# Kernel optimization log

Hardware: AMD Instinct MI355X
Metric: run time of the kernel (lower is better)

Reference implementation:

```python
import jax, jax.numpy as jnp
import numpy as np


def setup_inputs() -> dict:
    key = jax.random.key(0)
    k1, k2, k3, k4 = jax.random.split(key, 4)
    B, H, N, D = 4, 16, 2048, 128
    return {
        "q": jax.random.normal(k1, (B, H, N, D), dtype=jnp.float32),
        "k": jax.random.normal(k2, (B, H, N, D), dtype=jnp.float32),
        "v": jax.random.normal(k3, (B, H, N, D), dtype=jnp.float32),
        "g": jax.random.normal(k4, (B, H, N, 1), dtype=jnp.float32),
    }


def reference(q, k, v, g):
    """GLA recurrence: S_t = l_t * S_{t-1} + (1 - l_t) * k_t v_t^T; o_t = q_t S_t."""
    scale = 1.0
    B, H, N, D = q.shape
    lambd = jax.nn.sigmoid(g)                      # [B,H,N,1]
    qs = q * scale
    # time-major for scan: [N,B,H,...]
    qt = jnp.moveaxis(qs, 2, 0)
    kt = jnp.moveaxis(k, 2, 0)
    vt = jnp.moveaxis(v, 2, 0)
    lt = jnp.moveaxis(lambd, 2, 0)[..., None]      # [N,B,H,1,1]
    S0 = jnp.zeros((B, H, D, D), dtype=q.dtype)

    def step(S, inp):
        q_t, k_t, v_t, l_t = inp
        kv = jnp.einsum('bhd,bhe->bhde', k_t, v_t)  # rank-1 update per head
        S = l_t * S + (1.0 - l_t) * kv
        o = jnp.einsum('bhd,bhde->bhe', q_t, S)
        return S, o

    _, outs = jax.lax.scan(step, S0, (qt, kt, vt, lt))  # outs: [N,B,H,D]
    return jnp.moveaxis(outs, 0, 2)                     # [B,H,N,D]
```

## Files before the change

kernel.cpp:

```cpp
#include <hip/hip_runtime.h>

#define NTOK 2048
#define DD   128
#define CHK  64
#define PCH  16
#define EW   32

typedef __attribute__((ext_vector_type(8))) short bf16x8;
typedef __attribute__((ext_vector_type(4))) float f32x4;
typedef unsigned short u16;

#define MFMA(a,b,c) __builtin_amdgcn_mfma_f32_16x16x32_bf16(a,b,c,0,0,0)

#define SBAR() do{ __builtin_amdgcn_sched_barrier(0); \
  asm volatile("s_waitcnt lgkmcnt(0)" ::: "memory"); \
  __builtin_amdgcn_s_barrier(); \
  __builtin_amdgcn_sched_barrier(0); }while(0)
#define VWAIT() do{ asm volatile("s_waitcnt vmcnt(0)" ::: "memory"); \
  __builtin_amdgcn_sched_barrier(0); }while(0)

__device__ __forceinline__ u16 f2bf(float f){
  union { float f; unsigned u; } x; x.f = f;
  return (u16)((x.u + 0x7fffu + ((x.u >> 16) & 1u)) >> 16);
}
__device__ __forceinline__ int swz(int r, int c, int re){
  int b = (r*re + c)*2;
  return b ^ ((r & 7) << 4);
}
__device__ __forceinline__ void lds_w1(u16* a, int r, int c, int re, u16 v){
  *(u16*)((char*)a + swz(r,c,re)) = v;
}
__device__ __forceinline__ void lds_w4(u16* a, int r, int c, int re, ushort4 v){
  *(ushort4*)((char*)a + swz(r,c,re)) = v;
}
__device__ __forceinline__ bf16x8 lds_r8(const u16* a, int r, int c, int re){
  return *(const bf16x8*)((const char*)a + swz(r,c,re));
}

__global__ __launch_bounds__(256) void gla_part(
    const float* __restrict__ Qg, const float* __restrict__ Kg,
    const float* __restrict__ Vg, const float* __restrict__ Gg,
    float* __restrict__ Og, float* __restrict__ Smid, float* __restrict__ Bpre)
{
  __shared__ u16 sKh [CHK*DD];
  __shared__ u16 sKhT[DD*CHK];
  __shared__ u16 sVT [EW*CHK];
  __shared__ u16 sST [EW*DD];
  __shared__ u16 sPb [CHK*CHK];

  const int tid = threadIdx.x;
  const int w = tid >> 6, l = tid & 63, lr = l & 15, lh = l >> 4;
  const int gid  = blockIdx.x;
  const int head = (gid & 7) | (((gid >> 6) & 7) << 3);
  const int e0   = ((gid >> 3) & 3) * EW;
  const int part = (gid >> 5) & 1;
  const int tbase = part * (PCH*CHK);

  const float* Qh = Qg + (size_t)head*NTOK*DD;
  const float* Kh = Kg + (size_t)head*NTOK*DD;
  const float* Vh = Vg + (size_t)head*NTOK*DD;
  const float* Gh = Gg + (size_t)head*NTOK;
  float* Oh = Og + (size_t)head*NTOK*DD;

  f32x4 S00 = {}, S01 = {}, S10 = {}, S11 = {};
  float4 kt[2][4];
  float4 vpre[2], qpre[8];
  float gst;

  const int q4 = (tid >> 4) * 4;
  const int j0 = tid & 15;

  auto loads = [&](int c){
    const int t0 = tbase + c*CHK;
    gst = Gh[t0 + l];
    #pragma unroll
    for (int t=0;t<2;++t){
      const float* kp = Kh + (size_t)(t0 + q4)*DD + (j0 + 16*t)*4;
      #pragma unroll
      for (int r=0;r<4;++r) kt[t][r] = *(const float4*)(kp + r*DD);
    }
    const float* vp = Vh + (size_t)(t0 + (tid>>2))*DD + e0 + 4*(tid&3);
    #pragma unroll
    for (int i=0;i<2;++i) vpre[i] = *(const float4*)(vp + 16*i);
    const float* qp = Qh + (size_t)(t0 + w*16 + lr)*DD + lh*8;
    #pragma unroll
    for (int i=0;i<4;++i){
      qpre[2*i]   = *(const float4*)(qp + 32*i);
      qpre[2*i+1] = *(const float4*)(qp + 32*i + 4);
    }
  };

  float cklr, cq, scc, bl63;
  auto scan = [&](){
    float li = 1.f/(1.f + expf(-gst));
    float x  = log2f(li);
    #pragma unroll
    for (int off=1; off<64; off<<=1){
      float y = __shfl_up(x, off, 64);
      if (l >= off) x += y;
    }
    bl63 = __shfl(x, 63, 64);
    scc  = exp2f(bl63);
    cq   = exp2f(__shfl(x, w*16 + lr, 64));
    cklr = exp2f(-x) * (1.f - li);
  };

  loads(0);
  scan();
  float bsum = 0.f;
  if (part == 1 && e0 == 0 && tid == 0) Bpre[head*PCH] = 0.f;

  for (int c=0; c<PCH; ++c){
    SBAR();
    VWAIT();

    {
      const float cs0 = __shfl(cklr, q4+0, 64);
      const float cs1 = __shfl(cklr, q4+1, 64);
      const float cs2 = __shfl(cklr, q4+2, 64);
      const float cs3 = __shfl(cklr, q4+3, 64);
      #pragma unroll
      for (int t=0;t<2;++t){
        const int d0 = (j0 + 16*t)*4;
        ushort4 r0 = make_ushort4(f2bf(kt[t][0].x*cs0), f2bf(kt[t][0].y*cs0), f2bf(kt[t][0].z*cs0), f2bf(kt[t][0].w*cs0));
        ushort4 r1 = make_ushort4(f2bf(kt[t][1].x*cs1), f2bf(kt[t][1].y*cs1), f2bf(kt[t][1].z*cs1), f2bf(kt[t][1].w*cs1));
        ushort4 r2 = make_ushort4(f2bf(kt[t][2].x*cs2), f2bf(kt[t][2].y*cs2), f2bf(kt[t][2].z*cs2), f2bf(kt[t][2].w*cs2));
        ushort4 r3 = make_ushort4(f2bf(kt[t][3].x*cs3), f2bf(kt[t][3].y*cs3), f2bf(kt[t][3].z*cs3), f2bf(kt[t][3].w*cs3));
        lds_w4(sKh, q4+0, d0, DD, r0);
        lds_w4(sKh, q4+1, d0, DD, r1);
        lds_w4(sKh, q4+2, d0, DD, r2);
        lds_w4(sKh, q4+3, d0, DD, r3);
        lds_w4(sKhT, d0+0, q4, CHK, make_ushort4(r0.x, r1.x, r2.x, r3.x));
        lds_w4(sKhT, d0+1, q4, CHK, make_ushort4(r0.y, r1.y, r2.y, r3.y));
        lds_w4(sKhT, d0+2, q4, CHK, make_ushort4(r0.z, r1.z, r2.z, r3.z));
        lds_w4(sKhT, d0+3, q4, CHK, make_ushort4(r0.w, r1.w, r2.w, r3.w));
      }
    }
    {
      const int srow = tid >> 2;
      #pragma unroll
      for (int i=0;i<2;++i){
        float4 vf = vpre[i];
        int e = 4*((tid & 3) + 4*i);
        lds_w1(sVT, e+0, srow, CHK, f2bf(vf.x));
        lds_w1(sVT, e+1, srow, CHK, f2bf(vf.y));
        lds_w1(sVT, e+2, srow, CHK, f2bf(vf.z));
        lds_w1(sVT, e+3, srow, CHK, f2bf(vf.w));
      }
    }
    {
      const int dbase = w*32 + lh*4;
      lds_w4(sST, lr,    dbase,      DD, make_ushort4(f2bf(S00[0]), f2bf(S00[1]), f2bf(S00[2]), f2bf(S00[3])));
      lds_w4(sST, 16+lr, dbase,      DD, make_ushort4(f2bf(S01[0]), f2bf(S01[1]), f2bf(S01[2]), f2bf(S01[3])));
      lds_w4(sST, lr,    dbase + 16, DD, make_ushort4(f2bf(S10[0]), f2bf(S10[1]), f2bf(S10[2]), f2bf(S10[3])));
      lds_w4(sST, 16+lr, dbase + 16, DD, make_ushort4(f2bf(S11[0]), f2bf(S11[1]), f2bf(S11[2]), f2bf(S11[3])));
    }
    bf16x8 qA[4];
    #pragma unroll
    for (int ks=0;ks<4;++ks){
      float4 a = qpre[2*ks], b = qpre[2*ks+1];
      bf16x8 t;
      t[0]=(short)f2bf(a.x*cq); t[1]=(short)f2bf(a.y*cq);
      t[2]=(short)f2bf(a.z*cq); t[3]=(short)f2bf(a.w*cq);
      t[4]=(short)f2bf(b.x*cq); t[5]=(short)f2bf(b.y*cq);
      t[6]=(short)f2bf(b.z*cq); t[7]=(short)f2bf(b.w*cq);
      qA[ks] = t;
    }
    if (c+1 < PCH) loads(c+1);
    SBAR();

    f32x4 oacc0 = {}, oacc1 = {};
    f32x4 p0 = {}, p1 = {}, p2 = {}, p3 = {};
    #pragma unroll
    for (int ks=0;ks<4;++ks){
      const int kk = ks*32 + lh*8;
      bf16x8 a = qA[ks];
      oacc0 = MFMA(a, lds_r8(sST, lr,    kk, DD), oacc0);
      oacc1 = MFMA(a, lds_r8(sST, 16+lr, kk, DD), oacc1);
      p0 = MFMA(a, lds_r8(sKh, lr,    kk, DD), p0);
      p1 = MFMA(a, lds_r8(sKh, 16+lr, kk, DD), p1);
      p2 = MFMA(a, lds_r8(sKh, 32+lr, kk, DD), p2);
      p3 = MFMA(a, lds_r8(sKh, 48+lr, kk, DD), p3);
    }
    {
      const int t = w*16 + lh*4;
      #pragma unroll
      for (int r=0;r<4;++r){
        int tt = t + r;
        lds_w1(sPb, tt, lr,    CHK, f2bf((lr    <= tt) ? p0[r] : 0.f));
        lds_w1(sPb, tt, 16+lr, CHK, f2bf((16+lr <= tt) ? p1[r] : 0.f));
        lds_w1(sPb, tt, 32+lr, CHK, f2bf((32+lr <= tt) ? p2[r] : 0.f));
        lds_w1(sPb, tt, 48+lr, CHK, f2bf((48+lr <= tt) ? p3[r] : 0.f));
      }
    }
    asm volatile("s_waitcnt lgkmcnt(0)" ::: "memory");
    __builtin_amdgcn_sched_barrier(0);

    #pragma unroll
    for (int k2=0;k2<2;++k2){
      const int kk = k2*32 + lh*8;
      bf16x8 vb0 = lds_r8(sVT, lr,    kk, CHK);
      bf16x8 vb1 = lds_r8(sVT, 16+lr, kk, CHK);
      bf16x8 pa  = lds_r8(sPb, w*16 + lr, kk, CHK);
      oacc0 = MFMA(pa, vb0, oacc0);
      oacc1 = MFMA(pa, vb1, oacc1);
      bf16x8 ka0 = lds_r8(sKhT, w*32 + lr,      kk, CHK);
      bf16x8 ka1 = lds_r8(sKhT, w*32 + 16 + lr, kk, CHK);
      S00 = MFMA(ka0, vb0, S00);
      S01 = MFMA(ka0, vb1, S01);
      S10 = MFMA(ka1, vb0, S10);
      S11 = MFMA(ka1, vb1, S11);
    }
    #pragma unroll
    for (int r=0;r<4;++r){ S00[r]*=scc; S01[r]*=scc; S10[r]*=scc; S11[r]*=scc; }

    {
      float* op = Oh + (size_t)(tbase + c*CHK + w*16 + lh*4)*DD + e0;
      #pragma unroll
      for (int r=0;r<4;++r){
        op[r*DD + lr]      = oacc0[r];
        op[r*DD + 16 + lr] = oacc1[r];
      }
    }
    if (c+1 < PCH){
      if (part == 1){
        bsum += bl63;
        if (e0 == 0 && tid == 0) Bpre[head*PCH + c + 1] = bsum;
      }
      scan();
    }
  }

  if (part == 0){
    float* sm = Smid + (size_t)head*DD*DD + e0;
    const int dbase = w*32 + lh*4;
    #pragma unroll
    for (int r=0;r<4;++r){
      sm[(size_t)(dbase + r)*DD + lr]           = S00[r];
      sm[(size_t)(dbase + r)*DD + 16 + lr]      = S01[r];
      sm[(size_t)(dbase + 16 + r)*DD + lr]      = S10[r];
      sm[(size_t)(dbase + 16 + r)*DD + 16 + lr] = S11[r];
    }
  }
}

__global__ __launch_bounds__(256) void gla_fix(
    const float* __restrict__ Qg, const float* __restrict__ Gg,
    float* __restrict__ Og, const float* __restrict__ Smid,
    const float* __restrict__ Bpre)
{
  __shared__ u16 sS[DD*DD];
  const int tid = threadIdx.x;
  const int w = tid >> 6, l = tid & 63, lr = l & 15, lh = l >> 4;
  const int head = blockIdx.x >> 4, c = blockIdx.x & 15;
  const int t0 = PCH*CHK + c*CHK;

  {
    const int d = tid >> 1, eb = (tid & 1)*64;
    const float* sp = Smid + (size_t)head*DD*DD + (size_t)d*DD + eb;
    #pragma unroll
    for (int j=0;j<16;++j){
      float4 f = *(const float4*)(sp + 4*j);
      lds_w1(sS, eb + 4*j + 0, d, DD, f2bf(f.x));
      lds_w1(sS, eb + 4*j + 1, d, DD, f2bf(f.y));
      lds_w1(sS, eb + 4*j + 2, d, DD, f2bf(f.z));
      lds_w1(sS, eb + 4*j + 3, d, DD, f2bf(f.w));
    }
  }
  float gst = Gg[(size_t)head*NTOK + t0 + l];
  float li = 1.f/(1.f + expf(-gst));
  float x  = log2f(li);
  #pragma unroll
  for (int off=1; off<64; off<<=1){
    float y = __shfl_up(x, off, 64);
    if (l >= off) x += y;
  }
  const float cq = exp2f(__shfl(x, w*16 + lr, 64) + Bpre[head*PCH + c]);

  bf16x8 qA[4];
  const float* qp = Qg + (size_t)head*NTOK*DD + (size_t)(t0 + w*16 + lr)*DD + lh*8;
  #pragma unroll
  for (int ks=0;ks<4;++ks){
    float4 a = *(const float4*)(qp + ks*32);
    float4 b = *(const float4*)(qp + ks*32 + 4);
    bf16x8 t;
    t[0]=(short)f2bf(a.x*cq); t[1]=(short)f2bf(a.y*cq);
    t[2]=(short)f2bf(a.z*cq); t[3]=(short)f2bf(a.w*cq);
    t[4]=(short)f2bf(b.x*cq); t[5]=(short)f2bf(b.y*cq);
    t[6]=(short)f2bf(b.z*cq); t[7]=(short)f2bf(b.w*cq);
    qA[ks] = t;
  }
  __syncthreads();

  f32x4 o0={},o1={},o2={},o3={},o4={},o5={},o6={},o7={};
  #pragma unroll
  for (int ks=0;ks<4;++ks){
    const int kk = ks*32 + lh*8;
    bf16x8 a = qA[ks];
    o0 = MFMA(a, lds_r8(sS, lr,      kk, DD), o0);
    o1 = MFMA(a, lds_r8(sS, 16+lr,   kk, DD), o1);
    o2 = MFMA(a, lds_r8(sS, 32+lr,   kk, DD), o2);
    o3 = MFMA(a, lds_r8(sS, 48+lr,   kk, DD), o3);
    o4 = MFMA(a, lds_r8(sS, 64+lr,   kk, DD), o4);
    o5 = MFMA(a, lds_r8(sS, 80+lr,   kk, DD), o5);
    o6 = MFMA(a, lds_r8(sS, 96+lr,   kk, DD), o6);
    o7 = MFMA(a, lds_r8(sS, 112+lr,  kk, DD), o7);
  }
  float* op = Og + (size_t)head*NTOK*DD + (size_t)(t0 + w*16 + lh*4)*DD;
  #pragma unroll
  for (int r=0;r<4;++r){
    op[r*DD + lr]       += o0[r];
    op[r*DD + 16 + lr]  += o1[r];
    op[r*DD + 32 + lr]  += o2[r];
    op[r*DD + 48 + lr]  += o3[r];
    op[r*DD + 64 + lr]  += o4[r];
    op[r*DD + 80 + lr]  += o5[r];
    op[r*DD + 96 + lr]  += o6[r];
    op[r*DD + 112 + lr] += o7[r];
  }
}

extern "C" void kernel_launch(void* const* d_in, const int* in_sizes, int n_in,
                              void* d_out, int out_size, void* d_ws, size_t ws_size,
                              hipStream_t stream)
{
  const float* q = (const float*)d_in[0];
  const float* k = (const float*)d_in[1];
  const float* v = (const float*)d_in[2];
  const float* g = (const float*)d_in[3];
  float* out = (float*)d_out;
  float* Smid = (float*)d_ws;
  float* Bpre = (float*)((char*)d_ws + (size_t)64*DD*DD*4);

  gla_part<<<dim3(512),  dim3(256), 0, stream>>>(q, k, v, g, out, Smid, Bpre);
  gla_fix <<<dim3(1024), dim3(256), 0, stream>>>(q, g, out, Smid, Bpre);
}
```

Before: 140.6 us.

## Split sequence into four parts and combine partial states in fixup

New measurement: 177.9 us. +26.5%, slower.

```diff
diff --git a/kernel.cpp b/kernel.cpp
--- a/kernel.cpp
+++ b/kernel.cpp
@@ -1,10 +1,12 @@
 #include <hip/hip_runtime.h>
 
 #define NTOK 2048
-#define DD   128
-#define CHK  64
-#define PCH  16
-#define EW   32
+#define DD    128
+#define CHK   64
+#define NPART 4
+#define PCH   8
+#define EW    32
+#define SEL   16384
 
 typedef __attribute__((ext_vector_type(8))) short bf16x8;
 typedef __attribute__((ext_vector_type(4))) float f32x4;
@@ -40,7 +42,8 @@
 __global__ __launch_bounds__(256) void gla_part(
     const float* __restrict__ Qg, const float* __restrict__ Kg,
     const float* __restrict__ Vg, const float* __restrict__ Gg,
-    float* __restrict__ Og, float* __restrict__ Smid, float* __restrict__ Bpre)
+    float* __restrict__ Og, float* __restrict__ Umid,
+    float* __restrict__ Btot, float* __restrict__ Bpre)
 {
   __shared__ u16 sKh [CHK*DD];
   __shared__ u16 sKhT[DD*CHK];
@@ -51,9 +54,9 @@
   const int tid = threadIdx.x;
   const int w = tid >> 6, l = tid & 63, lr = l & 15, lh = l >> 4;
   const int gid  = blockIdx.x;
-  const int head = (gid & 7) | (((gid >> 6) & 7) << 3);
+  const int head = (gid & 7) | (((gid >> 7) & 7) << 3);
   const int e0   = ((gid >> 3) & 3) * EW;
-  const int part = (gid >> 5) & 1;
+  const int part = (gid >> 5) & 3;
   const int tbase = part * (PCH*CHK);
 
   const float* Qh = Qg + (size_t)head*NTOK*DD;
@@ -108,7 +111,7 @@
   loads(0);
   scan();
   float bsum = 0.f;
-  if (part == 1 && e0 == 0 && tid == 0) Bpre[head*PCH] = 0.f;
+  if (e0 == 0 && tid == 0) Bpre[head*(NPART*PCH) + part*PCH] = 0.f;
 
   for (int c=0; c<PCH; ++c){
     SBAR();
@@ -223,16 +226,15 @@
       }
     }
     if (c+1 < PCH){
-      if (part == 1){
-        bsum += bl63;
-        if (e0 == 0 && tid == 0) Bpre[head*PCH + c + 1] = bsum;
-      }
+      bsum += bl63;
+      if (e0 == 0 && tid == 0) Bpre[head*(NPART*PCH) + part*PCH + c + 1] = bsum;
       scan();
     }
   }
-
-  if (part == 0){
-    float* sm = Smid + (size_t)head*DD*DD + e0;
+  bsum += bl63;
+
+  if (part < 3){
+    float* sm = Umid + ((size_t)head*3 + part)*SEL + e0;
     const int dbase = w*32 + lh*4;
     #pragma unroll
     for (int r=0;r<4;++r){
@@ -242,29 +244,44 @@
       sm[(size_t)(dbase + 16 + r)*DD + 16 + lr] = S11[r];
     }
   }
+  if ((part == 1 || part == 2) && e0 == 0 && tid == 0)
+    Btot[head*NPART + part] = bsum;
 }
 
 __global__ __launch_bounds__(256) void gla_fix(
     const float* __restrict__ Qg, const float* __restrict__ Gg,
-    float* __restrict__ Og, const float* __restrict__ Smid,
-    const float* __restrict__ Bpre)
+    float* __restrict__ Og, const float* __restrict__ Umid,
+    const float* __restrict__ Btot, const float* __restrict__ Bpre)
 {
   __shared__ u16 sS[DD*DD];
   const int tid = threadIdx.x;
   const int w = tid >> 6, l = tid & 63, lr = l & 15, lh = l >> 4;
-  const int head = blockIdx.x >> 4, c = blockIdx.x & 15;
-  const int t0 = PCH*CHK + c*CHK;
+  const int head = blockIdx.x & 63, ci = blockIdx.x >> 6;
+  const int p = 1 + (ci >> 3), cwp = ci & 7;
+  const int t0 = p*(PCH*CHK) + cwp*CHK;
 
   {
     const int d = tid >> 1, eb = (tid & 1)*64;
-    const float* sp = Smid + (size_t)head*DD*DD + (size_t)d*DD + eb;
+    const float* u0 = Umid + (size_t)head*3*SEL + (size_t)d*DD + eb;
+    const float a1 = exp2f(Btot[head*NPART + 1]);
+    const float a2 = exp2f(Btot[head*NPART + 2]);
     #pragma unroll
     for (int j=0;j<16;++j){
-      float4 f = *(const float4*)(sp + 4*j);
-      lds_w1(sS, eb + 4*j + 0, d, DD, f2bf(f.x));
-      lds_w1(sS, eb + 4*j + 1, d, DD, f2bf(f.y));
-      lds_w1(sS, eb + 4*j + 2, d, DD, f2bf(f.z));
-      lds_w1(sS, eb + 4*j + 3, d, DD, f2bf(f.w));
+      float4 s = *(const float4*)(u0 + 4*j);
+      if (p >= 2){
+        float4 u1 = *(const float4*)(u0 + SEL + 4*j);
+        s.x = fmaf(a1, s.x, u1.x); s.y = fmaf(a1, s.y, u1.y);
+        s.z = fmaf(a1, s.z, u1.z); s.w = fmaf(a1, s.w, u1.w);
+      }
+      if (p == 3){
+        float4 u2 = *(const float4*)(u0 + 2*SEL + 4*j);
+        s.x = fmaf(a2, s.x, u2.x); s.y = fmaf(a2, s.y, u2.y);
+        s.z = fmaf(a2, s.z, u2.z); s.w = fmaf(a2, s.w, u2.w);
+      }
+      lds_w1(sS, eb + 4*j + 0, d, DD, f2bf(s.x));
+      lds_w1(sS, eb + 4*j + 1, d, DD, f2bf(s.y));
+      lds_w1(sS, eb + 4*j + 2, d, DD, f2bf(s.z));
+      lds_w1(sS, eb + 4*j + 3, d, DD, f2bf(s.w));
     }
   }
   float gst = Gg[(size_t)head*NTOK + t0 + l];
@@ -275,7 +292,7 @@
     float y = __shfl_up(x, off, 64);
     if (l >= off) x += y;
   }
-  const float cq = exp2f(__shfl(x, w*16 + lr, 64) + Bpre[head*PCH + c]);
+  const float cq = exp2f(__shfl(x, w*16 + lr, 64) + Bpre[head*(NPART*PCH) + p*PCH + cwp]);
 
   bf16x8 qA[4];
   const float* qp = Qg + (size_t)head*NTOK*DD + (size_t)(t0 + w*16 + lr)*DD + lh*8;
@@ -329,9 +346,12 @@
   const float* v = (const float*)d_in[2];
   const float* g = (const float*)d_in[3];
   float* out = (float*)d_out;
-  float* Smid = (float*)d_ws;
-  float* Bpre = (float*)((char*)d_ws + (size_t)64*DD*DD*4);
-
-  gla_part<<<dim3(512),  dim3(256), 0, stream>>>(q, k, v, g, out, Smid, Bpre);
-  gla_fix <<<dim3(1024), dim3(256), 0, stream>>>(q, g, out, Smid, Bpre);
-}
+
+  char* ws = (char*)d_ws;
+  float* Umid = (float*)ws;
+  float* Btot = (float*)(ws + 12582912);
+  float* Bpre = (float*)(ws + 12583936);
+
+  gla_part<<<dim3(1024), dim3(256), 0, stream>>>(q, k, v, g, out, Umid, Btot, Bpre);
+  gla_fix <<<dim3(1536), dim3(256), 0, stream>>>(q, g, out, Umid, Btot, Bpre);
+}
```
